# Kernel optimization log

Hardware: AMD Instinct MI355X
Metric: run time of the kernel (lower is better)

The kernel has to match this reference:

```python
import jax, jax.numpy as jnp
import numpy as np

B, C, L, H = 2, 512, 4096, 8
D = C // H  # depth per head


def setup_inputs() -> dict:
    key = jax.random.key(0)
    k1, k2, k3 = jax.random.split(key, 3)
    queries = jax.random.normal(k1, (B, C, L), dtype=jnp.float32)
    mask = jnp.ones((B, L), dtype=jnp.int32)
    # xavier-ish scaling for stability
    Wm = jax.random.normal(k2, (2 * C, C), dtype=jnp.float32) * (1.0 / np.sqrt(C))
    Wq = jax.random.normal(k3, (C, C), dtype=jnp.float32) * (1.0 / np.sqrt(C))
    return {"queries": queries, "mask": mask, "Wm": Wm, "Wq": Wq}


def reference(queries, mask, Wm, Wq):
    # 1x1 conv projections == channel matmuls on [B, C, L]
    q = jnp.einsum('oc,bcl->bol', Wq, queries)   # [B, C, L]
    m = jnp.einsum('oc,bcl->bol', Wm, queries)   # [B, 2C, L]
    # to [B, L, *], split heads -> [B, H, L, D]
    qh = q.transpose(0, 2, 1).reshape(B, L, H, D).transpose(0, 2, 1, 3)
    mem = m.transpose(0, 2, 1)                   # [B, L, 2C]
    k, v = jnp.split(mem, 2, axis=2)             # each [B, L, C]
    kh = k.reshape(B, L, H, D).transpose(0, 2, 1, 3)
    vh = v.reshape(B, L, H, D).transpose(0, 2, 1, 3)
    qh = qh * (D ** -0.5)
    logits = jnp.einsum('bhqd,bhkd->bhqk', qh, kh)          # [B, H, L, L]
    mf = mask.astype(jnp.float32)[:, None, None, :]          # [B, 1, 1, L]
    logits = logits + (-1e30) * (1.0 - mf)
    weights = jax.nn.softmax(logits, axis=-1)                # dropout is identity in eval
    out = jnp.einsum('bhqk,bhkd->bhqd', weights, vh)         # [B, H, L, D]
    # combine heads -> [B, L, C] -> [B, C, L]
    return out.transpose(0, 2, 1, 3).reshape(B, L, C).transpose(0, 2, 1)
```

## Files before the change

### kernel.cpp

```cpp
#include <hip/hip_runtime.h>

#define Bn 2
#define Cn 512
#define Ln 4096
#define Hn 8
#define Dn 64

typedef _Float16 f16;
typedef _Float16 h8 __attribute__((ext_vector_type(8)));
typedef _Float16 h4 __attribute__((ext_vector_type(4)));
typedef float f32x4 __attribute__((ext_vector_type(4)));
typedef float f32x16 __attribute__((ext_vector_type(16)));

#define MFMA32(a, b, c) __builtin_amdgcn_mfma_f32_16x16x32_f16(a, b, c, 0, 0, 0)
#define MFMA3216(a, b, c) __builtin_amdgcn_mfma_f32_32x32x16_f16(a, b, c, 0, 0, 0)
#define AS1(p) ((const __attribute__((address_space(1))) void*)(p))
#define AS3(p) ((__attribute__((address_space(3))) void*)(p))

__global__ __launch_bounds__(256) void k_transpose(const float* __restrict__ X,
                                                   f16* __restrict__ Xt) {
  int bid = blockIdx.x;
  int b  = bid >> 9;
  int r  = bid & 511;
  int lt = r >> 3, ct = r & 7;
  int l0 = lt << 6, c0 = ct << 6;
  __shared__ f16 t[64][66];
  int tid = threadIdx.x;
  int lx = tid & 63, cg = tid >> 6;
  const float* xb = X + ((size_t)b * Cn) * Ln;
#pragma unroll
  for (int rr = 0; rr < 16; ++rr) {
    int cl = cg * 16 + rr;
    t[lx][cl] = (f16)xb[(size_t)(c0 + cl) * Ln + l0 + lx];
  }
  __syncthreads();
  f16* xo = Xt + ((size_t)b * Ln + l0) * Cn + c0;
  int cx = tid & 63, lg = tid >> 6;
#pragma unroll
  for (int rr = 0; rr < 16; ++rr) {
    int ll = lg * 16 + rr;
    xo[(size_t)ll * Cn + cx] = t[ll][cx];
  }
}

__global__ __launch_bounds__(256) void k_proj(const float* __restrict__ Wq,
                                              const float* __restrict__ Wm,
                                              const f16* __restrict__ Xt,
                                              f16* __restrict__ Qd,
                                              f16* __restrict__ Kd,
                                              f16* __restrict__ Vv) {
  int bid = blockIdx.x;
  int b = bid / 384;
  int r = bid % 384;
  int mt = r >> 5, nt = r & 31;
  int o0 = mt << 7, l0 = nt << 7;
  __shared__ f16 a_lds[128][40];
  __shared__ f16 b_lds[128][40];
  int tid = threadIdx.x;
  int lane = tid & 63, w = tid >> 6;
  int wr = w >> 1, wc = w & 1;
  f32x4 acc[4][4] = {};

  int sr = tid >> 1;
  int scg = (tid & 1) << 4;
  int o_s = o0 + sr;
  const float* wrow = (o_s < 512) ? (Wq + (size_t)o_s * Cn)
                                  : (Wm + (size_t)(o_s - 512) * Cn);
  const f16* xrow = Xt + ((size_t)b * Ln + l0 + sr) * Cn;

  for (int kt = 0; kt < 16; ++kt) {
    int c0 = kt << 5;
    __syncthreads();
#pragma unroll
    for (int i = 0; i < 4; ++i) {
      float4 w4 = *(const float4*)(wrow + c0 + scg + 4 * i);
      h4 hh = { (f16)w4.x, (f16)w4.y, (f16)w4.z, (f16)w4.w };
      *(h4*)&a_lds[sr][scg + 4 * i] = hh;
    }
#pragma unroll
    for (int i = 0; i < 2; ++i)
      *(h8*)&b_lds[sr][scg + 8 * i] = *(const h8*)(xrow + c0 + scg + 8 * i);
    __syncthreads();

    h8 af[4], bf[4];
#pragma unroll
    for (int mi = 0; mi < 4; ++mi)
      af[mi] = *(const h8*)&a_lds[wr * 64 + mi * 16 + (lane & 15)][(lane >> 4) * 8];
#pragma unroll
    for (int ni = 0; ni < 4; ++ni)
      bf[ni] = *(const h8*)&b_lds[wc * 64 + ni * 16 + (lane & 15)][(lane >> 4) * 8];
#pragma unroll
    for (int mi = 0; mi < 4; ++mi)
#pragma unroll
      for (int ni = 0; ni < 4; ++ni)
        acc[mi][ni] = MFMA32(af[mi], bf[ni], acc[mi][ni]);
  }

  const float QSCALE = 0.18033688011112042f;
  int lrow = (lane >> 4) << 2;
  int lcol = lane & 15;
#pragma unroll
  for (int mi = 0; mi < 4; ++mi) {
    int ob = o0 + wr * 64 + mi * 16 + lrow;
#pragma unroll
    for (int ni = 0; ni < 4; ++ni) {
      int lc = l0 + wc * 64 + ni * 16 + lcol;
      f32x4 a = acc[mi][ni];
      if (ob < 512) {
        int h = ob >> 6, d = ob & 63;
        h4 hh = { (f16)(a[0] * QSCALE), (f16)(a[1] * QSCALE),
                  (f16)(a[2] * QSCALE), (f16)(a[3] * QSCALE) };
        *(h4*)&Qd[(((size_t)b * Hn + h) * Ln + lc) * Dn + d] = hh;
      } else if (ob < 1024) {
        int oc = ob - 512;
        int h = oc >> 6, d = oc & 63;
        h4 hh = { (f16)a[0], (f16)a[1], (f16)a[2], (f16)a[3] };
        *(h4*)&Kd[(((size_t)b * Hn + h) * Ln + lc) * Dn + d] = hh;
      } else {
        int oc = ob - 1024;
#pragma unroll
        for (int rr = 0; rr < 4; ++rr)
          Vv[((size_t)b * Cn + oc + rr) * Ln + lc] = (f16)a[rr];
      }
    }
  }
}

__global__ __launch_bounds__(512, 4) void k_attn(const f16* __restrict__ Qd,
                                                 const f16* __restrict__ Kd,
                                                 const f16* __restrict__ Vv,
                                                 const int* __restrict__ mask,
                                                 float* __restrict__ out) {
  int bid0 = blockIdx.x;
  int bid = (bid0 & 7) * 64 + (bid0 >> 3);
  int bh = bid >> 5, ib = bid & 31;
  int b = bh >> 3, h = bh & 7;
  int tid = threadIdx.x;
  int lane = tid & 63, w = tid >> 6;
  int grp = w >> 2, wq = w & 3;
  int il = lane & 31, hi = lane >> 5;

  __shared__ __align__(16) f16 smem[8 * 4096];
#define KBUF(g, bi) (&smem[(((g) * 2 + (bi))) * 4096])
#define VBUF(g, bi) (&smem[((4 + (g) * 2 + (bi))) * 4096])

  int qb = ib * 128 + wq * 32;
  const f16* qp = Qd + ((size_t)bh * Ln + qb + il) * Dn;
  h8 qreg[4];
#pragma unroll
  for (int dt = 0; dt < 4; ++dt)
    qreg[dt] = *(const h8*)(qp + dt * 16 + hi * 8);

  const int* mbase = mask + (size_t)b * Ln;
  unsigned long long flags;
  {
    const int4* mp = (const int4*)mbase + lane * 16;
    int ac = 1;
#pragma unroll
    for (int q = 0; q < 16; ++q) { int4 v = mp[q]; ac &= v.x & v.y & v.z & v.w; }
    flags = __ballot(ac == 1);
  }

  const f16* kbase = Kd + (size_t)bh * Ln * Dn + (size_t)grp * 32 * 4096;
  const f16* vbase = Vv + ((size_t)b * Cn + h * 64) * Ln + grp * 32 * 64;
  int koff[2], voff[2];
#pragma unroll
  for (int q = 0; q < 2; ++q) {
    int rr = wq * 16 + q * 8 + (lane >> 3);
    int swz = (lane & 7) ^ (rr & 7);
    koff[q] = rr * 64 + swz * 8;
    voff[q] = rr * Ln + swz * 8;
  }

#define STAGE(bi, t)                                                            \
  {                                                                             \
    _Pragma("unroll")                                                           \
    for (int q = 0; q < 2; ++q) {                                               \
      __builtin_amdgcn_global_load_lds(AS1(kbase + (size_t)(t) * 4096 + koff[q]),\
                                       AS3(KBUF(grp, bi) + (wq * 16 + q * 8) * 64),\
                                       16, 0, 0);                               \
      __builtin_amdgcn_global_load_lds(AS1(vbase + (size_t)(t) * 64 + voff[q]), \
                                       AS3(VBUF(grp, bi) + (wq * 16 + q * 8) * 64),\
                                       16, 0, 0);                               \
    }                                                                           \
  }

#define PACK_PB(S0_, S1_, DW0_, DW1_, PB_)                                      \
  {                                                                             \
    _Pragma("unroll")                                                           \
    for (int r = 0; r < 16; r += 2) {                                           \
      DW0_[r >> 1] = __builtin_bit_cast(float,                                  \
          __builtin_amdgcn_cvt_pkrtz(S0_[r], S0_[r + 1]));                      \
      DW1_[r >> 1] = __builtin_bit_cast(float,                                  \
          __builtin_amdgcn_cvt_pkrtz(S1_[r], S1_[r + 1]));                      \
    }                                                                           \
    _Pragma("unroll")                                                           \
    for (int jt = 0; jt < 4; ++jt) {                                            \
      float* dd = (jt < 2) ? DW0_ : DW1_;                                       \
      int base = (jt & 1) * 4;                                                  \
      float a0 = dd[base + 0], b0 = dd[base + 2];                               \
      float a1 = dd[base + 1], b1 = dd[base + 3];                               \
      asm("v_permlane32_swap_b32 %0, %1" : "+v"(a0), "+v"(b0));                 \
      asm("v_permlane32_swap_b32 %0, %1" : "+v"(a1), "+v"(b1));                 \
      union { h8 v; float f[4]; } u;                                            \
      u.f[0] = a0; u.f[1] = a1; u.f[2] = b0; u.f[3] = b1;                       \
      PB_[jt] = u.v;                                                            \
    }                                                                           \
  }

  f32x16 acc0 = {}, acc1 = {};
  float mrow = 0.f;
  float lsum = 0.f;
  int swz7 = il & 7;

  STAGE(0, 0);
  STAGE(1, 1);

#define BODY(t_, waitn_)                                                        \
  {                                                                             \
    asm volatile("s_waitcnt vmcnt(" waitn_ ")" ::: "memory");                   \
    __builtin_amdgcn_s_barrier();                                               \
    const f16* kl_ = KBUF(grp, (t_) & 1);                                       \
    f32x16 s0 = {}, s1 = {};                                                    \
    __builtin_amdgcn_s_setprio(1);                                              \
    _Pragma("unroll")                                                           \
    for (int dt = 0; dt < 4; ++dt) {                                            \
      int c = ((dt * 2 + hi) ^ swz7) << 3;                                      \
      h8 ak0 = *(const h8*)&kl_[il * 64 + c];                                   \
      h8 ak1 = *(const h8*)&kl_[(32 + il) * 64 + c];                            \
      s0 = MFMA3216(ak0, qreg[dt], s0);                                         \
      s1 = MFMA3216(ak1, qreg[dt], s1);                                         \
    }                                                                           \
    __builtin_amdgcn_s_setprio(0);                                              \
    int T_ = grp * 32 + (t_);                                                   \
    if (!((flags >> T_) & 1)) {                                                 \
      _Pragma("unroll")                                                         \
      for (int r = 0; r < 16; ++r) {                                            \
        int j = T_ * 64 + (r & 3) + 8 * (r >> 2) + 4 * hi;                      \
        if (!mbase[j])      s0[r] = -3.0e4f;                                    \
        if (!mbase[j + 32]) s1[r] = -3.0e4f;                                    \
      }                                                                         \
    }                                                                           \
    _Pragma("unroll")                                                           \
    for (int r = 0; r < 16; ++r) {                                              \
      s0[r] = __builtin_amdgcn_exp2f(s0[r] - mrow);                             \
      s1[r] = __builtin_amdgcn_exp2f(s1[r] - mrow);                             \
    }                                                                           \
    float dw0[8], dw1[8];                                                       \
    h8 pb[4];                                                                   \
    PACK_PB(s0, s1, dw0, dw1, pb);                                              \
    float rs;                                                                   \
    {                   \
      float a0 = (s0[0] + s0[1]) + (s0[2] + s0[3]);                             \
      float a1 = (s0[4] + s0[5]) + (s0[6] + s0[7]);                             \
      float a2 = (s0[8] + s0[9]) + (s0[10] + s0[11]);                           \
      float a3 = (s0[12] + s0[13]) + (s0[14] + s0[15]);                         \
      float a4 = (s1[0] + s1[1]) + (s1[2] + s1[3]);                             \
      float a5 = (s1[4] + s1[5]) + (s1[6] + s1[7]);                             \
      float a6 = (s1[8] + s1[9]) + (s1[10] + s1[11]);                           \
      float a7 = (s1[12] + s1[13]) + (s1[14] + s1[15]);                         \
      rs = ((a0 + a1) + (a2 + a3)) + ((a4 + a5) + (a6 + a7));                   \
    }                                                                           \
    if (__any(rs > 8192.f)) {   \
      float mxp = fmaxf(                                                        \
        fmaxf(fmaxf(fmaxf(s0[0], s0[1]), fmaxf(s0[2], s0[3])),                  \
              fmaxf(fmaxf(s0[4], s0[5]), fmaxf(s0[6], s0[7]))),                 \
        fmaxf(fmaxf(fmaxf(s0[8], s0[9]), fmaxf(s0[10], s0[11])),                \
              fmaxf(fmaxf(s0[12], s0[13]), fmaxf(s0[14], s0[15]))));            \
      float mxq = fmaxf(                                                        \
        fmaxf(fmaxf(fmaxf(s1[0], s1[1]), fmaxf(s1[2], s1[3])),                  \
              fmaxf(fmaxf(s1[4], s1[5]), fmaxf(s1[6], s1[7]))),                 \
        fmaxf(fmaxf(fmaxf(s1[8], s1[9]), fmaxf(s1[10], s1[11])),                \
              fmaxf(fmaxf(s1[12], s1[13]), fmaxf(s1[14], s1[15]))));            \
      mxp = fmaxf(mxp, mxq);                                                    \
      mxp = fmaxf(mxp, __shfl_xor(mxp, 32));                   \
      int e = (((__builtin_bit_cast(int, mxp) >> 23) & 255) - 127) - 3;         \
      float sc = __builtin_bit_cast(float, (127 - e) << 23);    \
      mrow += (float)e;                                                         \
      _Pragma("unroll")                                                         \
      for (int r = 0; r < 16; ++r) {                                            \
        s0[r] *= sc; s1[r] *= sc;                                               \
        acc0[r] *= sc; acc1[r] *= sc;                                           \
      }                                                                         \
      lsum *= sc; rs *= sc;                                                     \
      PACK_PB(s0, s1, dw0, dw1, pb);                                            \
    }                                                                           \
    lsum += rs;                                                                 \
    const f16* vl_ = VBUF(grp, (t_) & 1);                                       \
    __builtin_amdgcn_s_setprio(1);                                              \
    _Pragma("unroll")                                                           \
    for (int dt = 0; dt < 2; ++dt) {                                            \
      int rv = dt * 32 + il;                                                    \
      _Pragma("unroll")                                                         \
      for (int jt = 0; jt < 4; ++jt) {                                          \
        h8 av = *(const h8*)&vl_[rv * 64 + (((jt * 2 + hi) ^ swz7) << 3)];      \
        if (dt == 0) acc0 = MFMA3216(av, pb[jt], acc0);                         \
        else         acc1 = MFMA3216(av, pb[jt], acc1);                         \
      }                                                                         \
    }                                                                           \
    __builtin_amdgcn_s_setprio(0);                                              \
    __builtin_amdgcn_s_barrier();                                               \
    if ((t_) < 30) STAGE((t_) & 1, (t_) + 2);                                   \
  }

  for (int t = 0; t < 31; ++t) {
    BODY(t, "4");
  }
  BODY(31, "0");

  lsum += __shfl_xor(lsum, 32);

  __syncthreads();
  float* shf = (float*)smem;
  if (grp == 1) {
    float* basep = shf + wq * (64 * 33) + lane * 33;
#pragma unroll
    for (int r = 0; r < 16; ++r) { basep[r] = acc0[r]; basep[16 + r] = acc1[r]; }
    float* ml = shf + 4 * 64 * 33 + (wq * 64 + lane) * 2;
    ml[0] = mrow; ml[1] = lsum;
  }
  __syncthreads();
  if (grp == 0) {
    float* basep = shf + wq * (64 * 33) + lane * 33;
    float* ml = shf + 4 * 64 * 33 + (wq * 64 + lane) * 2;
    float mB = ml[0], lB = ml[1];
    float M = fmaxf(mrow, mB);
    float wA = __builtin_amdgcn_exp2f(mrow - M);
    float wB = __builtin_amdgcn_exp2f(mB - M);
    float linv = 1.f / fmaxf(lsum * wA + lB * wB, 1e-30f);
    float fA = wA * linv, fB = wB * linv;
    size_t obase = ((size_t)b * Cn + h * 64) * Ln + qb + il;
#pragma unroll
    for (int r = 0; r < 16; ++r) {
      int d0 = (r & 3) + 8 * (r >> 2) + 4 * hi;
      out[obase + (size_t)d0 * Ln] = acc0[r] * fA + basep[r] * fB;
      out[obase + (size_t)(d0 + 32) * Ln] = acc1[r] * fA + basep[16 + r] * fB;
    }
  }
}

extern "C" void kernel_launch(void* const* d_in, const int* in_sizes, int n_in,
                              void* d_out, int out_size, void* d_ws, size_t ws_size,
                              hipStream_t stream) {
  const float* queries = (const float*)d_in[0];
  const int*   mask    = (const int*)d_in[1];
  const float* Wm      = (const float*)d_in[2];
  const float* Wq      = (const float*)d_in[3];
  float* out = (float*)d_out;
  char* ws = (char*)d_ws;
  f16* Xt = (f16*)(ws);
  f16* Qd = (f16*)(ws + 8388608);
  f16* Kd = (f16*)(ws + 16777216);
  f16* Vv = (f16*)(ws + 25165824);

  k_transpose<<<1024, 256, 0, stream>>>(queries, Xt);
  k_proj<<<768, 256, 0, stream>>>(Wq, Wm, Xt, Qd, Kd, Vv);
  k_attn<<<512, 512, 0, stream>>>(Qd, Kd, Vv, mask, out);
}
```

Measured before the change: 137.3 us.

## Software-pipeline QK of next tile with softmax and PV of previous tile

The attention loop is restructured so each iteration computes the QK^T scores for tile t while running softmax and the PV MFMAs for tile t-1, holding two sets of score registers that alternate. K and V staging are split so the next K tile is loaded before QK and the next V tile after PV, with a lighter vmcnt wait and a separate prologue and epilogue. The aim is to overlap MFMA work with exp/pack VALU work and with global-to-LDS loads. The cost is 32 extra live float registers per thread, which may raise register pressure or lower occupancy.

```diff
diff --git a/kernel.cpp b/kernel.cpp
--- a/kernel.cpp
+++ b/kernel.cpp
@@ -172,17 +172,21 @@
     voff[q] = rr * Ln + swz * 8;
   }
 
-#define STAGE(bi, t)                                                            \
-  {                                                                             \
-    _Pragma("unroll")                                                           \
-    for (int q = 0; q < 2; ++q) {                                               \
+#define STAGE_K(bi, t)                                                          \
+  {                                                                             \
+    _Pragma("unroll")                                                           \
+    for (int q = 0; q < 2; ++q)                                                 \
       __builtin_amdgcn_global_load_lds(AS1(kbase + (size_t)(t) * 4096 + koff[q]),\
                                        AS3(KBUF(grp, bi) + (wq * 16 + q * 8) * 64),\
                                        16, 0, 0);                               \
+  }
+#define STAGE_V(bi, t)                                                          \
+  {                                                                             \
+    _Pragma("unroll")                                                           \
+    for (int q = 0; q < 2; ++q)                                                 \
       __builtin_amdgcn_global_load_lds(AS1(vbase + (size_t)(t) * 64 + voff[q]), \
                                        AS3(VBUF(grp, bi) + (wq * 16 + q * 8) * 64),\
                                        16, 0, 0);                               \
-    }                                                                           \
   }
 
 #define PACK_PB(S0_, S1_, DW0_, DW1_, PB_)                                      \
@@ -213,23 +217,18 @@
   float lsum = 0.f;
   int swz7 = il & 7;
 
-  STAGE(0, 0);
-  STAGE(1, 1);
-
-#define BODY(t_, waitn_)                                                        \
-  {                                                                             \
-    asm volatile("s_waitcnt vmcnt(" waitn_ ")" ::: "memory");                   \
-    __builtin_amdgcn_s_barrier();                                               \
+#define QK(t_, S0_, S1_)                                                        \
+  {                                                                             \
     const f16* kl_ = KBUF(grp, (t_) & 1);                                       \
-    f32x16 s0 = {}, s1 = {};                                                    \
+    f32x16 z0 = {}, z1 = {};                                                    \
     __builtin_amdgcn_s_setprio(1);                                              \
     _Pragma("unroll")                                                           \
     for (int dt = 0; dt < 4; ++dt) {                                            \
       int c = ((dt * 2 + hi) ^ swz7) << 3;                                      \
       h8 ak0 = *(const h8*)&kl_[il * 64 + c];                                   \
       h8 ak1 = *(const h8*)&kl_[(32 + il) * 64 + c];                            \
-      s0 = MFMA3216(ak0, qreg[dt], s0);                                         \
-      s1 = MFMA3216(ak1, qreg[dt], s1);                                         \
+      z0 = MFMA3216(ak0, qreg[dt], z0);                                         \
+      z1 = MFMA3216(ak1, qreg[dt], z1);                                         \
     }                                                                           \
     __builtin_amdgcn_s_setprio(0);                                              \
     int T_ = grp * 32 + (t_);                                                   \
@@ -237,53 +236,58 @@
       _Pragma("unroll")                                                         \
       for (int r = 0; r < 16; ++r) {                                            \
         int j = T_ * 64 + (r & 3) + 8 * (r >> 2) + 4 * hi;                      \
-        if (!mbase[j])      s0[r] = -3.0e4f;                                    \
-        if (!mbase[j + 32]) s1[r] = -3.0e4f;                                    \
+        if (!mbase[j])      z0[r] = -3.0e4f;                                    \
+        if (!mbase[j + 32]) z1[r] = -3.0e4f;                                    \
       }                                                                         \
     }                                                                           \
+    S0_ = z0; S1_ = z1;                                                         \
+  }
+
+#define SM_PV(t_, S0_, S1_)                                                     \
+  {                                                                             \
     _Pragma("unroll")                                                           \
     for (int r = 0; r < 16; ++r) {                                              \
-      s0[r] = __builtin_amdgcn_exp2f(s0[r] - mrow);                             \
-      s1[r] = __builtin_amdgcn_exp2f(s1[r] - mrow);                             \
+      S0_[r] = __builtin_amdgcn_exp2f(S0_[r] - mrow);                           \
+      S1_[r] = __builtin_amdgcn_exp2f(S1_[r] - mrow);                           \
     }                                                                           \
     float dw0[8], dw1[8];                                                       \
     h8 pb[4];                                                                   \
-    PACK_PB(s0, s1, dw0, dw1, pb);                                              \
+    PACK_PB(S0_, S1_, dw0, dw1, pb);                                            \
     float rs;                                                                   \
-    {                   \
-      float a0 = (s0[0] + s0[1]) + (s0[2] + s0[3]);                             \
-      float a1 = (s0[4] + s0[5]) + (s0[6] + s0[7]);                             \
-      float a2 = (s0[8] + s0[9]) + (s0[10] + s0[11]);                           \
-      float a3 = (s0[12] + s0[13]) + (s0[14] + s0[15]);                         \
-      float a4 = (s1[0] + s1[1]) + (s1[2] + s1[3]);                             \
-      float a5 = (s1[4] + s1[5]) + (s1[6] + s1[7]);                             \
-      float a6 = (s1[8] + s1[9]) + (s1[10] + s1[11]);                           \
-      float a7 = (s1[12] + s1[13]) + (s1[14] + s1[15]);                         \
+    {                                                                           \
+      float a0 = (S0_[0] + S0_[1]) + (S0_[2] + S0_[3]);                         \
+      float a1 = (S0_[4] + S0_[5]) + (S0_[6] + S0_[7]);                         \
+      float a2 = (S0_[8] + S0_[9]) + (S0_[10] + S0_[11]);                       \
+      float a3 = (S0_[12] + S0_[13]) + (S0_[14] + S0_[15]);                     \
+      float a4 = (S1_[0] + S1_[1]) + (S1_[2] + S1_[3]);                         \
+      float a5 = (S1_[4] + S1_[5]) + (S1_[6] + S1_[7]);                         \
+      float a6 = (S1_[8] + S1_[9]) + (S1_[10] + S1_[11]);                       \
+      float a7 = (S1_[12] + S1_[13]) + (S1_[14] + S1_[15]);                     \
       rs = ((a0 + a1) + (a2 + a3)) + ((a4 + a5) + (a6 + a7));                   \
     }                                                                           \
-    if (__any(rs > 8192.f)) {   \
+    if (__any(rs > 8192.f)) {    \
       float mxp = fmaxf(                                                        \
-        fmaxf(fmaxf(fmaxf(s0[0], s0[1]), fmaxf(s0[2], s0[3])),                  \
-              fmaxf(fmaxf(s0[4], s0[5]), fmaxf(s0[6], s0[7]))),                 \
-        fmaxf(fmaxf(fmaxf(s0[8], s0[9]), fmaxf(s0[10], s0[11])),                \
-              fmaxf(fmaxf(s0[12], s0[13]), fmaxf(s0[14], s0[15]))));            \
+        fmaxf(fmaxf(fmaxf(S0_[0], S0_[1]), fmaxf(S0_[2], S0_[3])),              \
+              fmaxf(fmaxf(S0_[4], S0_[5]), fmaxf(S0_[6], S0_[7]))),             \
+        fmaxf(fmaxf(fmaxf(S0_[8], S0_[9]), fmaxf(S0_[10], S0_[11])),            \
+              fmaxf(fmaxf(S0_[12], S0_[13]), fmaxf(S0_[14], S0_[15]))));        \
       float mxq = fmaxf(                                                        \
-        fmaxf(fmaxf(fmaxf(s1[0], s1[1]), fmaxf(s1[2], s1[3])),                  \
-              fmaxf(fmaxf(s1[4], s1[5]), fmaxf(s1[6], s1[7]))),                 \
-        fmaxf(fmaxf(fmaxf(s1[8], s1[9]), fmaxf(s1[10], s1[11])),                \
-              fmaxf(fmaxf(s1[12], s1[13]), fmaxf(s1[14], s1[15]))));            \
+        fmaxf(fmaxf(fmaxf(S1_[0], S1_[1]), fmaxf(S1_[2], S1_[3])),              \
+              fmaxf(fmaxf(S1_[4], S1_[5]), fmaxf(S1_[6], S1_[7]))),             \
+        fmaxf(fmaxf(fmaxf(S1_[8], S1_[9]), fmaxf(S1_[10], S1_[11])),            \
+              fmaxf(fmaxf(S1_[12], S1_[13]), fmaxf(S1_[14], S1_[15]))));        \
       mxp = fmaxf(mxp, mxq);                                                    \
-      mxp = fmaxf(mxp, __shfl_xor(mxp, 32));                   \
+      mxp = fmaxf(mxp, __shfl_xor(mxp, 32));                                    \
       int e = (((__builtin_bit_cast(int, mxp) >> 23) & 255) - 127) - 3;         \
-      float sc = __builtin_bit_cast(float, (127 - e) << 23);    \
+      float sc = __builtin_bit_cast(float, (127 - e) << 23);          \
       mrow += (float)e;                                                         \
       _Pragma("unroll")                                                         \
       for (int r = 0; r < 16; ++r) {                                            \
-        s0[r] *= sc; s1[r] *= sc;                                               \
+        S0_[r] *= sc; S1_[r] *= sc;                                             \
         acc0[r] *= sc; acc1[r] *= sc;                                           \
       }                                                                         \
       lsum *= sc; rs *= sc;                                                     \
-      PACK_PB(s0, s1, dw0, dw1, pb);                                            \
+      PACK_PB(S0_, S1_, dw0, dw1, pb);                                          \
     }                                                                           \
     lsum += rs;                                                                 \
     const f16* vl_ = VBUF(grp, (t_) & 1);                                       \
@@ -299,14 +303,37 @@
       }                                                                         \
     }                                                                           \
     __builtin_amdgcn_s_setprio(0);                                              \
+  }
+
+#define BODYR(t_, SN0, SN1, SP0, SP1)                                           \
+  {                                                                             \
+    asm volatile("s_waitcnt vmcnt(1)" ::: "memory");   \
     __builtin_amdgcn_s_barrier();                                               \
-    if ((t_) < 30) STAGE((t_) & 1, (t_) + 2);                                   \
-  }
-
-  for (int t = 0; t < 31; ++t) {
-    BODY(t, "4");
-  }
-  BODY(31, "0");
+    if ((t_) + 1 < 32) STAGE_K(((t_) + 1) & 1, (t_) + 1);                       \
+    QK(t_, SN0, SN1);                                                           \
+    SM_PV((t_) - 1, SP0, SP1);                                                  \
+    __builtin_amdgcn_s_barrier();                                               \
+    if ((t_) + 1 < 32) STAGE_V(((t_) + 1) & 1, (t_) + 1);                       \
+  }
+
+  f32x16 sE0, sE1, sO0, sO1;
+
+  STAGE_K(0, 0);
+  STAGE_V(0, 0);
+  asm volatile("s_waitcnt vmcnt(0)" ::: "memory");
+  __builtin_amdgcn_s_barrier();
+  STAGE_K(1, 1);
+  QK(0, sE0, sE1);
+  __builtin_amdgcn_s_barrier();
+  STAGE_V(1, 1);
+
+  for (int t = 1; t < 31; t += 2) {
+    BODYR(t, sO0, sO1, sE0, sE1);
+    BODYR(t + 1, sE0, sE1, sO0, sO1);
+  }
+  BODYR(31, sO0, sO1, sE0, sE1);
+  asm volatile("s_waitcnt vmcnt(0)" ::: "memory");
+  SM_PV(31, sO0, sO1);
 
   lsum += __shfl_xor(lsum, 32);
 
```

Result: slower. 474.0 us (+245.3%).
